# Optimization experiments

Hardware: AMD Instinct MI355X
Metric: run time of the kernel (lower is better)

The kernel has to match this reference:

```python
import jax, jax.numpy as jnp
import numpy as np

DIM = 2048
N_HEADS = 32
N_KV_HEADS = 8
HEAD_DIM = 64
REPEATS = N_HEADS // N_KV_HEADS
SLIDING_WINDOW = 1024
EPS = 1e-6
B, T = 2, 2048


def _alibi_slopes(n):
    # n_heads=32 is a power of 2
    r = 2.0 ** (-8.0 / n)
    return jnp.asarray([r ** i for i in range(n)], dtype=jnp.float32)


def _rms_norm(x, w, eps):
    # RMSNorm over the last (flattened heads*head_dim) axis
    var = jnp.mean(x * x, axis=-1, keepdims=True)
    return x * jax.lax.rsqrt(var + eps) * w


def setup_inputs() -> dict:
    key = jax.random.key(0)
    ks = jax.random.split(key, 6)
    s = 0.02
    return {
        "x": jax.random.normal(ks[0], (B, T, DIM), jnp.float32),
        "wq": jax.random.normal(ks[1], (N_HEADS * HEAD_DIM, DIM), jnp.float32) * s,
        "wk": jax.random.normal(ks[2], (N_KV_HEADS * HEAD_DIM, DIM), jnp.float32) * s,
        "wv": jax.random.normal(ks[3], (N_KV_HEADS * HEAD_DIM, DIM), jnp.float32) * s,
        "wo": jax.random.normal(ks[4], (DIM, N_HEADS * HEAD_DIM), jnp.float32) * s,
        "q_norm_w": jnp.ones((N_HEADS * HEAD_DIM,), jnp.float32),
        "k_norm_w": jnp.ones((N_KV_HEADS * HEAD_DIM,), jnp.float32),
    }


def reference(x, wq, wk, wv, wo, q_norm_w, k_norm_w):
    bsz, seqlen, _ = x.shape
    xq = _rms_norm(x @ wq.T, q_norm_w, EPS)
    xk = _rms_norm(x @ wk.T, k_norm_w, EPS)
    xv = x @ wv.T
    xq = xq.reshape(bsz, seqlen, N_HEADS, HEAD_DIM).transpose(0, 2, 1, 3)  # b h t d
    xk = xk.reshape(bsz, seqlen, N_KV_HEADS, HEAD_DIM).transpose(0, 2, 1, 3)
    xv = xv.reshape(bsz, seqlen, N_KV_HEADS, HEAD_DIM).transpose(0, 2, 1, 3)
    # GQA: repeat_interleave kv heads
    xk = jnp.repeat(xk, REPEATS, axis=1)
    xv = jnp.repeat(xv, REPEATS, axis=1)

    pos = jnp.arange(seqlen)
    dist = pos[None, :] - pos[:, None]                     # [t,s] = s - t (<=0 on causal side)
    slopes = _alibi_slopes(N_HEADS)
    alibi = slopes[:, None, None] * dist.astype(jnp.float32)  # [h,t,s]
    allowed = (dist <= 0) & (dist >= -SLIDING_WINDOW)      # causal + sliding window
    bias = jnp.where(allowed[None], alibi, -jnp.inf)       # [h,t,s]

    scale = 1.0 / jnp.sqrt(jnp.asarray(HEAD_DIM, jnp.float32))
    scores = jnp.einsum("bhtd,bhsd->bhts", xq, xk) * scale + bias[None]
    attn = jax.nn.softmax(scores, axis=-1)
    out = jnp.einsum("bhts,bhsd->bhtd", attn, xv)          # [b,h,t,d]
    out = out.transpose(0, 2, 1, 3).reshape(bsz, seqlen, N_HEADS * HEAD_DIM)
    return out @ wo.T
```

## Files before the change

### kernel.cpp

```cpp
#include <hip/hip_runtime.h>


typedef _Float16 f16;
typedef __attribute__((ext_vector_type(8))) _Float16 f16x8;
typedef __attribute__((ext_vector_type(4))) _Float16 f16x4;
typedef __attribute__((ext_vector_type(2))) _Float16 f16x2;
typedef __attribute__((ext_vector_type(4))) float f32x4;

#define T_ 2048
#define NH 32
#define NKV 8
#define HD 64
#define WINDOW 1024
#define EPS_ 1e-6f
#define LOG2E 1.44269504088896340736f
#define LDQKV 3072

__device__ inline void async16(void* lds, const void* g) {
  __builtin_amdgcn_global_load_lds(
      (const __attribute__((address_space(1))) unsigned int*)g,
      (__attribute__((address_space(3))) unsigned int*)lds, 16, 0, 0);
}

struct CvtArgs {
  const float* src[5];
  f16* dst[5];
  int n4[5];
};
__global__ __launch_bounds__(256) void cvt_multi(CvtArgs a) {
  const int seg = blockIdx.y;
  const float* in = a.src[seg];
  f16* out = a.dst[seg];
  const int n4 = a.n4[seg];
  for (int i = blockIdx.x * blockDim.x + threadIdx.x; i < n4;
       i += gridDim.x * blockDim.x) {
    float4 v = ((const float4*)in)[i];
    f16x4 o;
    o[0] = (f16)v.x; o[1] = (f16)v.y; o[2] = (f16)v.z; o[3] = (f16)v.w;
    ((f16x4*)out)[i] = o;
  }
}


#define DSRD(p, off) (*(const f16x8*)((p) + (off)))

template <int BN>
__global__ __launch_bounds__(512, 2) void gemm_nt8(const f16* __restrict__ A,
                                                   const f16* __restrict__ B,
                                                   void* __restrict__ C,
                                                   int M, int N, int K, int ldc,
                                                   int out_f32) {
  constexpr int WN = BN / 4;
  constexpr int JN = WN / 32;
  constexpr int RB = BN / 64;
  constexpr int BUFB = BN * 128;
  extern __shared__ char smem[];
  f16* sA = (f16*)smem;
  f16* sB = (f16*)(smem + 65536);

  const int gx = gridDim.x;
  const int nwg = gx * gridDim.y;
  int bid = blockIdx.y * gx + blockIdx.x;
  if (!(nwg & 7)) bid = (bid & 7) * (nwg >> 3) + (bid >> 3);
  const int m0 = (bid / gx) * 256;
  const int n0 = (bid % gx) * BN;

  const int tid = threadIdx.x;
  const int lane = tid & 63;
  const int wave = tid >> 6;
  const int quad = lane >> 4, l16 = lane & 15;
  const int wm = wave >> 2, wn = wave & 3;

  const int srow = tid >> 3;
  const int sgr = (((tid & 7) ^ (srow & 7))) * 8;
  const f16* gA = A + (size_t)(m0 + srow) * K + sgr;
  const f16* gB = B + (size_t)(n0 + srow) * K + sgr;
  const size_t r64 = (size_t)64 * K;

  const char* cA = (const char*)sA;
  const char* cB = (const char*)sB;
  const int xm = (l16 & 7) << 4;
  const int xk0 = (quad * 16) ^ xm;
  const int xk1 = (64 + quad * 16) ^ xm;
  const int abase = (wm * 128 + l16) * 128;
  const int bbase = (wn * WN + l16) * 128;

  f32x4 acc[8][2 * JN] = {};
  const int nt = K >> 6;

#pragma unroll
  for (int a = 0; a < 4; ++a)
    async16(sA + a * 4096 + tid * 8, gA + (size_t)a * r64);
#pragma unroll
  for (int rb = 0; rb < RB; ++rb)
    async16(sB + rb * 4096 + tid * 8, gB + (size_t)rb * r64);
  asm volatile("s_waitcnt vmcnt(0)" ::: "memory");
  __builtin_amdgcn_s_barrier();

  for (int t = 0; t < nt; ++t) {
    const int bufoA = (t & 1) << 15;
    const int bufoB = (t & 1) * BUFB;
    f16* sAn = sA + (((t & 1) ^ 1) << 14);
    f16* sBn = sB + ((t & 1) ^ 1) * (BUFB / 2);
    const bool st = (t + 1 < nt);
    const size_t gk = (size_t)(t + 1) * 64;

    f16x8 af[4][2], bf[JN][2];

    auto ldA = [&](int mh) {
#pragma unroll
      for (int i = 0; i < 4; ++i) {
        af[i][0] = DSRD(cA, bufoA + abase + mh * 8192 + i * 2048 + xk0);
        af[i][1] = DSRD(cA, bufoA + abase + mh * 8192 + i * 2048 + xk1);
      }
    };
    auto ldB = [&](int nh) {
#pragma unroll
      for (int j = 0; j < JN; ++j) {
        bf[j][0] = DSRD(cB, bufoB + bbase + nh * (WN / 2) * 128 + j * 2048 + xk0);
        bf[j][1] = DSRD(cB, bufoB + bbase + nh * (WN / 2) * 128 + j * 2048 + xk1);
      }
    };
    auto mm = [&](int mh, int nh) {
      __builtin_amdgcn_s_barrier();
      asm volatile("s_waitcnt lgkmcnt(0)" ::: "memory");
      __builtin_amdgcn_sched_barrier(0);
      __builtin_amdgcn_s_setprio(1);
#pragma unroll
      for (int i = 0; i < 4; ++i) {
#pragma unroll
        for (int j = 0; j < JN; ++j) {
          acc[mh * 4 + i][nh * JN + j] = __builtin_amdgcn_mfma_f32_16x16x32_f16(
              af[i][0], bf[j][0], acc[mh * 4 + i][nh * JN + j], 0, 0, 0);
          acc[mh * 4 + i][nh * JN + j] = __builtin_amdgcn_mfma_f32_16x16x32_f16(
              af[i][1], bf[j][1], acc[mh * 4 + i][nh * JN + j], 0, 0, 0);
        }
      }
      __builtin_amdgcn_s_setprio(0);
    };

    ldA(0); ldB(0);
    if (st) {
      async16(sAn + 0 * 4096 + tid * 8, gA + 0 * r64 + gk);
      async16(sAn + 1 * 4096 + tid * 8, gA + 1 * r64 + gk);
      async16(sBn + 0 * 4096 + tid * 8, gB + 0 * r64 + gk);
      if (RB == 4) async16(sBn + 1 * 4096 + tid * 8, gB + 1 * r64 + gk);
    }
    mm(0, 0);
    __builtin_amdgcn_s_barrier();

    ldB(1);
    if (st) {
      async16(sAn + 2 * 4096 + tid * 8, gA + 2 * r64 + gk);
      async16(sAn + 3 * 4096 + tid * 8, gA + 3 * r64 + gk);
      if (RB == 4) {
        async16(sBn + 2 * 4096 + tid * 8, gB + 2 * r64 + gk);
        async16(sBn + 3 * 4096 + tid * 8, gB + 3 * r64 + gk);
      } else {
        async16(sBn + 1 * 4096 + tid * 8, gB + 1 * r64 + gk);
      }
    }
    mm(0, 1);
    __builtin_amdgcn_s_barrier();

    ldA(1); ldB(0);
    mm(1, 0);
    __builtin_amdgcn_s_barrier();

    ldB(1);
    mm(1, 1);
    if (st) asm volatile("s_waitcnt vmcnt(0)" ::: "memory");
    __builtin_amdgcn_s_barrier();
  }

#pragma unroll
  for (int im = 0; im < 8; ++im) {
    const int row0 = m0 + wm * 128 + im * 16 + quad * 4;
#pragma unroll
    for (int jn = 0; jn < 2 * JN; ++jn) {
      const int col = n0 + wn * WN + jn * 16 + l16;
#pragma unroll
      for (int r = 0; r < 4; ++r) {
        const float v = acc[im][jn][r];
        if (out_f32) ((float*)C)[(size_t)(row0 + r) * ldc + col] = v;
        else         ((f16*)C)[(size_t)(row0 + r) * ldc + col] = (f16)v;
      }
    }
  }
}

__global__ __launch_bounds__(256) void rmsnorm2(f16* __restrict__ xqkv,
                                                const float* __restrict__ qw,
                                                const float* __restrict__ kw) {
  __shared__ float red[4];
  const int which = blockIdx.y;
  const int tid = threadIdx.x;

  auto block_sum = [&](float ss) -> float {
#pragma unroll
    for (int off = 32; off > 0; off >>= 1) ss += __shfl_down(ss, off);
    if ((tid & 63) == 0) red[tid >> 6] = ss;
    __syncthreads();
    return red[0] + red[1] + red[2] + red[3];
  };

  if (which == 0) {
    f16* p = xqkv + (size_t)blockIdx.x * LDQKV;
    f16x8 v = ((const f16x8*)p)[tid];
    float f[8];
    float ss = 0.f;
#pragma unroll
    for (int j = 0; j < 8; ++j) { f[j] = (float)v[j]; ss += f[j] * f[j]; }
    const float scale = rsqrtf(block_sum(ss) / 2048.0f + EPS_);
    const float4 w0 = ((const float4*)qw)[tid * 2];
    const float4 w1 = ((const float4*)qw)[tid * 2 + 1];
    f16x8 o;
    o[0] = (f16)(f[0] * scale * w0.x); o[1] = (f16)(f[1] * scale * w0.y);
    o[2] = (f16)(f[2] * scale * w0.z); o[3] = (f16)(f[3] * scale * w0.w);
    o[4] = (f16)(f[4] * scale * w1.x); o[5] = (f16)(f[5] * scale * w1.y);
    o[6] = (f16)(f[6] * scale * w1.z); o[7] = (f16)(f[7] * scale * w1.w);
    ((f16x8*)p)[tid] = o;
  } else {
    f16* p = xqkv + (size_t)blockIdx.x * LDQKV + 2048;
    f16x2 v = ((const f16x2*)p)[tid];
    const float f0 = (float)v[0], f1 = (float)v[1];
    const float scale = rsqrtf(block_sum(f0 * f0 + f1 * f1) / 512.0f + EPS_);
    const float2 w = ((const float2*)kw)[tid];
    f16x2 o;
    o[0] = (f16)(f0 * scale * w.x);
    o[1] = (f16)(f1 * scale * w.y);
    ((f16x2*)p)[tid] = o;
  }
}

__global__ __launch_bounds__(256) void kvfrag(const f16* __restrict__ xqkv,
                                              f16* __restrict__ Kf,
                                              f16* __restrict__ Vf) {
  __shared__ f16 Lk[64][72];
  __shared__ f16 Lv[64][72];
  const int kt = blockIdx.x;
  const int b = blockIdx.y >> 3, kh = blockIdx.y & 7;
  const int t0 = kt * 64;
  const int tid = threadIdx.x;
  const int r = tid >> 3, c = (tid & 7) * 8;
#pragma unroll
  for (int rp = 0; rp < 2; ++rp) {
    const int rr = r + rp * 32;
    const f16* src = xqkv + (size_t)(b * T_ + t0 + rr) * LDQKV + kh * 64 + c;
    *(f16x8*)(&Lk[rr][c]) = *(const f16x8*)(src + 2048);
    *(f16x8*)(&Lv[rr][c]) = *(const f16x8*)(src + 2560);
  }
  __syncthreads();
  const size_t obase = ((size_t)(b * 8 + kh) * 32 + kt) * 4096;
#pragma unroll
  for (int cc0 = 0; cc0 < 2; ++cc0) {
    const int cc = tid + cc0 * 256;
    const int nb = cc >> 7, kc = (cc >> 6) & 1, ln = cc & 63;
    const int qd = ln >> 4, s16 = ln & 15;
    *(f16x8*)(Kf + obase + cc * 8) = *(const f16x8*)(&Lk[nb * 16 + s16][kc * 32 + qd * 8]);
    f16x8 o;
#pragma unroll
    for (int j = 0; j < 8; ++j) o[j] = Lv[kc * 32 + qd * 8 + j][nb * 16 + s16];
    *(f16x8*)(Vf + obase + cc * 8) = o;
  }
}

__global__ __launch_bounds__(256, 8) void attn(const f16* __restrict__ Q,
                                               const f16* __restrict__ Kf,
                                               const f16* __restrict__ Vf,
                                               f16* __restrict__ O) {
  constexpr int LDW = 72;
  __shared__ f16 Qs[64 * LDW];
  __shared__ float Lx[4][16];

  const int qt = blockIdx.x, h = blockIdx.y, b = blockIdx.z;
  const int kh = h >> 2;
  const int q0 = qt * 64;
  const int tid = threadIdx.x;
  const int lane = tid & 63, wave = tid >> 6;
  const int quad = lane >> 4, l16 = lane & 15;
  const float scale2 = 0.125f * LOG2E;
  const float slope2 = exp2f(-0.25f * (float)h) * LOG2E;
  const float M2 = 10.0f;

  const int sr = tid >> 3, sc = (tid & 7) * 8;

#pragma unroll
  for (int rp = 0; rp < 2; ++rp) {
    const int rr = sr + rp * 32;
    *(f16x8*)(Qs + rr * LDW + sc) =
        *(const f16x8*)(Q + (size_t)(b * T_ + q0 + rr) * LDQKV + h * HD + sc);
  }
  __syncthreads();
  f16x8 qf[2];
#pragma unroll
  for (int kc = 0; kc < 2; ++kc)
    qf[kc] = *(const f16x8*)(Qs + (wave * 16 + l16) * LDW + kc * 32 + quad * 8);
  f16* Ps = Qs + wave * 16 * LDW;

  f32x4 o_acc[4] = {};
  float lsum = 0.f;

  const int kt_lo = (q0 >= WINDOW) ? ((q0 - WINDOW) >> 6) : 0;
  const int my_q = q0 + wave * 16 + l16;
  const f16* kfb = Kf + (size_t)(b * 8 + kh) * 131072 + lane * 8;
  const f16* vfb = Vf + (size_t)(b * 8 + kh) * 131072 + lane * 8;

  float sr4[4];
#pragma unroll
  for (int r = 0; r < 4; ++r) sr4[r] = slope2 * (float)r;
  float base = slope2 * (float)(kt_lo * 64 + quad * 4 - my_q) - M2;
  const float bstep = slope2 * 64.0f;
  const float b16 = slope2 * 16.0f;

  for (int kt = kt_lo; kt <= qt; ++kt) {
    const int k0 = kt * 64;
    const f16* kp = kfb + kt * 4096;
    const f16* vp = vfb + kt * 4096;
    const bool maskt = (kt == qt) || (q0 + 63 - k0 > WINDOW);

    float bnb = base;
#pragma unroll
    for (int nb = 0; nb < 4; ++nb) {
      f32x4 a = {0.f, 0.f, 0.f, 0.f};
#pragma unroll
      for (int kc = 0; kc < 2; ++kc) {
        const f16x8 kfr = *(const f16x8*)(kp + (nb * 2 + kc) * 512);
        a = __builtin_amdgcn_mfma_f32_16x16x32_f16(kfr, qf[kc], a, 0, 0, 0);
      }
      f16x4 pk;
#pragma unroll
      for (int r = 0; r < 4; ++r) {
        float v = fmaf(a[r], scale2, bnb + sr4[r]);
        if (maskt) {
          const int dist = k0 + nb * 16 + quad * 4 + r - my_q;
          if (dist > 0 || dist < -WINDOW) v = -1e30f;
        }
        const float p = __builtin_amdgcn_exp2f(v);
        lsum += p;
        pk[r] = (f16)p;
      }
      *(f16x4*)(Ps + l16 * LDW + nb * 16 + quad * 4) = pk;
      bnb += b16;
    }
    base += bstep;

#pragma unroll
    for (int nb = 0; nb < 4; ++nb) {
#pragma unroll
      for (int kc = 0; kc < 2; ++kc) {
        const f16x8 pa = *(const f16x8*)(Ps + l16 * LDW + kc * 32 + quad * 8);
        const f16x8 vb = *(const f16x8*)(vp + (nb * 2 + kc) * 512);
        o_acc[nb] = __builtin_amdgcn_mfma_f32_16x16x32_f16(pa, vb, o_acc[nb], 0, 0, 0);
      }
    }
  }

  lsum += __shfl_xor(lsum, 16);
  lsum += __shfl_xor(lsum, 32);
  if (quad == 0) Lx[wave][l16] = lsum;
  float rl[4];
#pragma unroll
  for (int r = 0; r < 4; ++r) rl[r] = 1.0f / Lx[wave][quad * 4 + r];

#pragma unroll
  for (int r = 0; r < 4; ++r) {
    const int q = q0 + wave * 16 + quad * 4 + r;
#pragma unroll
    for (int nb = 0; nb < 4; ++nb)
      O[(size_t)(b * T_ + q) * (NH * HD) + h * HD + nb * 16 + l16] =
          (f16)(o_acc[nb][r] * rl[r]);
  }
}

extern "C" void kernel_launch(void* const* d_in, const int* in_sizes, int n_in,
                              void* d_out, int out_size, void* d_ws, size_t ws_size,
                              hipStream_t stream) {
  const float* x  = (const float*)d_in[0];
  const float* wq = (const float*)d_in[1];
  const float* wk = (const float*)d_in[2];
  const float* wv = (const float*)d_in[3];
  const float* wo = (const float*)d_in[4];
  const float* qw = (const float*)d_in[5];
  const float* kw = (const float*)d_in[6];
  float* out = (float*)d_out;

  char* ws = (char*)d_ws;
  size_t off = 0;
  auto carve = [&](size_t bytes) -> char* {
    char* p = ws + off;
    off += (bytes + 255) & ~(size_t)255;
    return p;
  };
  f16* xh    = (f16*)carve((size_t)4096 * 2048 * 2);
  f16* wqkvh = (f16*)carve((size_t)3072 * 2048 * 2);
  f16* woh   = (f16*)carve((size_t)2048 * 2048 * 2);
  f16* xqkv  = (f16*)carve((size_t)4096 * 3072 * 2);
  f16* Kf = wqkvh;
  f16* Vf = wqkvh + (size_t)16 * 131072;
  f16* ao = xh;

  static bool attr_done = false;
  if (!attr_done) {
    (void)hipFuncSetAttribute((const void*)gemm_nt8<256>,
                              hipFuncAttributeMaxDynamicSharedMemorySize,
                              131072);
    (void)hipFuncSetAttribute((const void*)gemm_nt8<128>,
                              hipFuncAttributeMaxDynamicSharedMemorySize,
                              98304);
    attr_done = true;
  }

  CvtArgs ca;
  ca.src[0] = x;  ca.dst[0] = xh;                            ca.n4[0] = (4096 * 2048) / 4;
  ca.src[1] = wq; ca.dst[1] = wqkvh;                         ca.n4[1] = (2048 * 2048) / 4;
  ca.src[2] = wk; ca.dst[2] = wqkvh + (size_t)2048 * 2048;   ca.n4[2] = (512 * 2048) / 4;
  ca.src[3] = wv; ca.dst[3] = wqkvh + (size_t)2560 * 2048;   ca.n4[3] = (512 * 2048) / 4;
  ca.src[4] = wo; ca.dst[4] = woh;                           ca.n4[4] = (2048 * 2048) / 4;
  cvt_multi<<<dim3(1024, 5), 256, 0, stream>>>(ca);

  gemm_nt8<256><<<dim3(12, 16), 512, 131072, stream>>>(xh, wqkvh, xqkv, 4096, 3072, 2048, LDQKV, 0);
  rmsnorm2<<<dim3(4096, 2), 256, 0, stream>>>(xqkv, qw, kw);
  kvfrag<<<dim3(32, 16), 256, 0, stream>>>(xqkv, Kf, Vf);
  attn<<<dim3(32, 32, 2), 256, 0, stream>>>(xqkv, Kf, Vf, ao);
  gemm_nt8<128><<<dim3(16, 16), 512, 98304, stream>>>(ao, woh, out, 4096, 2048, 2048, 2048, 1);
}
```

Before: 315.7 us.

## Process two key tiles per iteration in attention with double P buffers

The attention loop is unrolled to handle two 64-key tiles per iteration, with a second LDS buffer for the P tile so the two tiles' QK MFMAs, softmax and PV MFMAs interleave for more instruction-level parallelism. It also adds s_setprio around the MFMA phases and splits the row-sum accumulator into four lanes. Launch bounds drop from 8 to 4 waves per SIMD, trading occupancy for registers. The mask logic is specialised (first tile of a pair only checks the window, second only the diagonal), which assumes pairs align to the diagonal.

New measurement: 353.7 us. 1.12x slower.

```diff
diff --git a/kernel.cpp b/kernel.cpp
--- a/kernel.cpp
+++ b/kernel.cpp
@@ -265,12 +265,13 @@
   }
 }
 
-__global__ __launch_bounds__(256, 8) void attn(const f16* __restrict__ Q,
+__global__ __launch_bounds__(256, 4) void attn(const f16* __restrict__ Q,
                                                const f16* __restrict__ Kf,
                                                const f16* __restrict__ Vf,
                                                f16* __restrict__ O) {
   constexpr int LDW = 72;
   __shared__ f16 Qs[64 * LDW];
+  __shared__ f16 P2s[64 * LDW];
   __shared__ float Lx[4][16];
 
   const int qt = blockIdx.x, h = blockIdx.y, b = blockIdx.z;
@@ -296,10 +297,11 @@
 #pragma unroll
   for (int kc = 0; kc < 2; ++kc)
     qf[kc] = *(const f16x8*)(Qs + (wave * 16 + l16) * LDW + kc * 32 + quad * 8);
-  f16* Ps = Qs + wave * 16 * LDW;
+  f16* PsA = Qs + wave * 16 * LDW;
+  f16* PsB = P2s + wave * 16 * LDW;
 
   f32x4 o_acc[4] = {};
-  float lsum = 0.f;
+  f32x4 lsum4 = {0.f, 0.f, 0.f, 0.f};
 
   const int kt_lo = (q0 >= WINDOW) ? ((q0 - WINDOW) >> 6) : 0;
   const int my_q = q0 + wave * 16 + l16;
@@ -311,51 +313,105 @@
   for (int r = 0; r < 4; ++r) sr4[r] = slope2 * (float)r;
   float base = slope2 * (float)(kt_lo * 64 + quad * 4 - my_q) - M2;
   const float bstep = slope2 * 64.0f;
-  const float b16 = slope2 * 16.0f;
-
-  for (int kt = kt_lo; kt <= qt; ++kt) {
-    const int k0 = kt * 64;
-    const f16* kp = kfb + kt * 4096;
-    const f16* vp = vfb + kt * 4096;
-    const bool maskt = (kt == qt) || (q0 + 63 - k0 > WINDOW);
-
-    float bnb = base;
+  const float b16s = slope2 * 16.0f;
+
+  auto smst = [&](const f32x4* s, bool maskt, int k0, float bb, f16* Pdst) {
+    float bnb = bb;
 #pragma unroll
     for (int nb = 0; nb < 4; ++nb) {
-      f32x4 a = {0.f, 0.f, 0.f, 0.f};
-#pragma unroll
-      for (int kc = 0; kc < 2; ++kc) {
-        const f16x8 kfr = *(const f16x8*)(kp + (nb * 2 + kc) * 512);
-        a = __builtin_amdgcn_mfma_f32_16x16x32_f16(kfr, qf[kc], a, 0, 0, 0);
-      }
       f16x4 pk;
 #pragma unroll
       for (int r = 0; r < 4; ++r) {
-        float v = fmaf(a[r], scale2, bnb + sr4[r]);
+        float v = fmaf(s[nb][r], scale2, bnb + sr4[r]);
         if (maskt) {
           const int dist = k0 + nb * 16 + quad * 4 + r - my_q;
           if (dist > 0 || dist < -WINDOW) v = -1e30f;
         }
         const float p = __builtin_amdgcn_exp2f(v);
-        lsum += p;
+        lsum4[r] += p;
         pk[r] = (f16)p;
       }
-      *(f16x4*)(Ps + l16 * LDW + nb * 16 + quad * 4) = pk;
-      bnb += b16;
-    }
-    base += bstep;
-
+      *(f16x4*)(Pdst + l16 * LDW + nb * 16 + quad * 4) = pk;
+      bnb += b16s;
+    }
+  };
+
+  int kt = kt_lo;
+  for (; kt + 1 <= qt; kt += 2) {
+    const int k0A = kt * 64, k0B = k0A + 64;
+    const f16* kpA = kfb + kt * 4096;
+    const f16* vpA = vfb + kt * 4096;
+
+    f32x4 sA[4], sB[4];
+    __builtin_amdgcn_s_setprio(1);
 #pragma unroll
     for (int nb = 0; nb < 4; ++nb) {
+      f32x4 a = {0.f, 0.f, 0.f, 0.f}, c = {0.f, 0.f, 0.f, 0.f};
 #pragma unroll
       for (int kc = 0; kc < 2; ++kc) {
-        const f16x8 pa = *(const f16x8*)(Ps + l16 * LDW + kc * 32 + quad * 8);
-        const f16x8 vb = *(const f16x8*)(vp + (nb * 2 + kc) * 512);
-        o_acc[nb] = __builtin_amdgcn_mfma_f32_16x16x32_f16(pa, vb, o_acc[nb], 0, 0, 0);
-      }
-    }
-  }
-
+        a = __builtin_amdgcn_mfma_f32_16x16x32_f16(
+            *(const f16x8*)(kpA + (nb * 2 + kc) * 512), qf[kc], a, 0, 0, 0);
+        c = __builtin_amdgcn_mfma_f32_16x16x32_f16(
+            *(const f16x8*)(kpA + 4096 + (nb * 2 + kc) * 512), qf[kc], c, 0, 0, 0);
+      }
+      sA[nb] = a; sB[nb] = c;
+    }
+    __builtin_amdgcn_s_setprio(0);
+
+    const bool maskA = (q0 + 63 - k0A > WINDOW);
+    const bool maskB = (k0B == q0);
+    smst(sA, maskA, k0A, base, PsA);
+    smst(sB, maskB, k0B, base + bstep, PsB);
+    base += 2.0f * bstep;
+
+    f16x8 paA[2], paB[2];
+#pragma unroll
+    for (int kc = 0; kc < 2; ++kc) {
+      paA[kc] = *(const f16x8*)(PsA + l16 * LDW + kc * 32 + quad * 8);
+      paB[kc] = *(const f16x8*)(PsB + l16 * LDW + kc * 32 + quad * 8);
+    }
+    __builtin_amdgcn_s_setprio(1);
+#pragma unroll
+    for (int nb = 0; nb < 4; ++nb) {
+#pragma unroll
+      for (int kc = 0; kc < 2; ++kc) {
+        o_acc[nb] = __builtin_amdgcn_mfma_f32_16x16x32_f16(
+            paA[kc], *(const f16x8*)(vpA + (nb * 2 + kc) * 512), o_acc[nb], 0, 0, 0);
+        o_acc[nb] = __builtin_amdgcn_mfma_f32_16x16x32_f16(
+            paB[kc], *(const f16x8*)(vpA + 4096 + (nb * 2 + kc) * 512), o_acc[nb], 0, 0, 0);
+      }
+    }
+    __builtin_amdgcn_s_setprio(0);
+  }
+
+  if (kt <= qt) {
+    const int k0 = kt * 64;
+    const f16* kp = kfb + kt * 4096;
+    const f16* vp = vfb + kt * 4096;
+    f32x4 s[4];
+#pragma unroll
+    for (int nb = 0; nb < 4; ++nb) {
+      f32x4 a = {0.f, 0.f, 0.f, 0.f};
+#pragma unroll
+      for (int kc = 0; kc < 2; ++kc)
+        a = __builtin_amdgcn_mfma_f32_16x16x32_f16(
+            *(const f16x8*)(kp + (nb * 2 + kc) * 512), qf[kc], a, 0, 0, 0);
+      s[nb] = a;
+    }
+    smst(s, true, k0, base, PsA);
+    f16x8 pa[2];
+#pragma unroll
+    for (int kc = 0; kc < 2; ++kc)
+      pa[kc] = *(const f16x8*)(PsA + l16 * LDW + kc * 32 + quad * 8);
+#pragma unroll
+    for (int nb = 0; nb < 4; ++nb)
+#pragma unroll
+      for (int kc = 0; kc < 2; ++kc)
+        o_acc[nb] = __builtin_amdgcn_mfma_f32_16x16x32_f16(
+            pa[kc], *(const f16x8*)(vp + (nb * 2 + kc) * 512), o_acc[nb], 0, 0, 0);
+  }
+
+  float lsum = lsum4[0] + lsum4[1] + lsum4[2] + lsum4[3];
   lsum += __shfl_xor(lsum, 16);
   lsum += __shfl_xor(lsum, 32);
   if (quad == 0) Lx[wave][l16] = lsum;
```

## Double-buffer K fragments in registers and reverse q-tile launch order

Applied to the files above, without the earlier changes.

Prefetches the next K tile's fragments into a second register buffer while the current tile is computed, so global load latency overlaps the MFMA and exp work. Launch bounds are relaxed from 8 to 4 blocks per SM to make room for the extra registers. Q-tiles are launched in reverse so the longest causal blocks start first, and the row-sum accumulator is split into four independent lanes to shorten the dependency chain. Lower occupancy may hurt latency hiding elsewhere in the kernel.

New measurement: 363.2 us. 15.1% more time.

```diff
diff --git a/kernel.cpp b/kernel.cpp
--- a/kernel.cpp
+++ b/kernel.cpp
@@ -265,7 +265,7 @@
   }
 }
 
-__global__ __launch_bounds__(256, 8) void attn(const f16* __restrict__ Q,
+__global__ __launch_bounds__(256, 4) void attn(const f16* __restrict__ Q,
                                                const f16* __restrict__ Kf,
                                                const f16* __restrict__ Vf,
                                                f16* __restrict__ O) {
@@ -273,7 +273,8 @@
   __shared__ f16 Qs[64 * LDW];
   __shared__ float Lx[4][16];
 
-  const int qt = blockIdx.x, h = blockIdx.y, b = blockIdx.z;
+  const int qt = 31 - blockIdx.x;
+  const int h = blockIdx.y, b = blockIdx.z;
   const int kh = h >> 2;
   const int q0 = qt * 64;
   const int tid = threadIdx.x;
@@ -299,7 +300,7 @@
   f16* Ps = Qs + wave * 16 * LDW;
 
   f32x4 o_acc[4] = {};
-  float lsum = 0.f;
+  f32x4 lsum4 = {0.f, 0.f, 0.f, 0.f};
 
   const int kt_lo = (q0 >= WINDOW) ? ((q0 - WINDOW) >> 6) : 0;
   const int my_q = q0 + wave * 16 + l16;
@@ -311,23 +312,28 @@
   for (int r = 0; r < 4; ++r) sr4[r] = slope2 * (float)r;
   float base = slope2 * (float)(kt_lo * 64 + quad * 4 - my_q) - M2;
   const float bstep = slope2 * 64.0f;
-  const float b16 = slope2 * 16.0f;
-
-  for (int kt = kt_lo; kt <= qt; ++kt) {
+  const float b16s = slope2 * 16.0f;
+
+  f16x8 kA[8], kB[8];
+  auto loadK = [&](f16x8 (&dst)[8], int kt2) {
+    const f16* kp = kfb + kt2 * 4096;
+#pragma unroll
+    for (int i = 0; i < 8; ++i) dst[i] = *(const f16x8*)(kp + i * 512);
+  };
+
+  auto body = [&](f16x8 (&cu)[8], f16x8 (&nx)[8], int kt) {
     const int k0 = kt * 64;
-    const f16* kp = kfb + kt * 4096;
+    if (kt < qt) loadK(nx, kt + 1);
+
+    const bool maskt = (kt == qt) || (q0 + 63 - k0 > WINDOW);
     const f16* vp = vfb + kt * 4096;
-    const bool maskt = (kt == qt) || (q0 + 63 - k0 > WINDOW);
-
     float bnb = base;
 #pragma unroll
     for (int nb = 0; nb < 4; ++nb) {
       f32x4 a = {0.f, 0.f, 0.f, 0.f};
 #pragma unroll
-      for (int kc = 0; kc < 2; ++kc) {
-        const f16x8 kfr = *(const f16x8*)(kp + (nb * 2 + kc) * 512);
-        a = __builtin_amdgcn_mfma_f32_16x16x32_f16(kfr, qf[kc], a, 0, 0, 0);
-      }
+      for (int kc = 0; kc < 2; ++kc)
+        a = __builtin_amdgcn_mfma_f32_16x16x32_f16(cu[nb * 2 + kc], qf[kc], a, 0, 0, 0);
       f16x4 pk;
 #pragma unroll
       for (int r = 0; r < 4; ++r) {
@@ -337,25 +343,34 @@
           if (dist > 0 || dist < -WINDOW) v = -1e30f;
         }
         const float p = __builtin_amdgcn_exp2f(v);
-        lsum += p;
+        lsum4[r] += p;
         pk[r] = (f16)p;
       }
       *(f16x4*)(Ps + l16 * LDW + nb * 16 + quad * 4) = pk;
-      bnb += b16;
+      bnb += b16s;
     }
     base += bstep;
 
-#pragma unroll
-    for (int nb = 0; nb < 4; ++nb) {
-#pragma unroll
-      for (int kc = 0; kc < 2; ++kc) {
-        const f16x8 pa = *(const f16x8*)(Ps + l16 * LDW + kc * 32 + quad * 8);
-        const f16x8 vb = *(const f16x8*)(vp + (nb * 2 + kc) * 512);
-        o_acc[nb] = __builtin_amdgcn_mfma_f32_16x16x32_f16(pa, vb, o_acc[nb], 0, 0, 0);
-      }
-    }
-  }
-
+    f16x8 pa[2];
+#pragma unroll
+    for (int kc = 0; kc < 2; ++kc)
+      pa[kc] = *(const f16x8*)(Ps + l16 * LDW + kc * 32 + quad * 8);
+#pragma unroll
+    for (int nb = 0; nb < 4; ++nb)
+#pragma unroll
+      for (int kc = 0; kc < 2; ++kc)
+        o_acc[nb] = __builtin_amdgcn_mfma_f32_16x16x32_f16(
+            pa[kc], *(const f16x8*)(vp + (nb * 2 + kc) * 512), o_acc[nb], 0, 0, 0);
+  };
+
+  loadK(kA, kt_lo);
+  int kt = kt_lo;
+  while (true) {
+    body(kA, kB, kt); if (++kt > qt) break;
+    body(kB, kA, kt); if (++kt > qt) break;
+  }
+
+  float lsum = lsum4[0] + lsum4[1] + lsum4[2] + lsum4[3];
   lsum += __shfl_xor(lsum, 16);
   lsum += __shfl_xor(lsum, 32);
   if (quad == 0) Lx[wave][l16] = lsum;
```
